# Performance work log

Measured on AMD Instinct MI355X. Metric: run time of the kernel, lower is better.

Reference implementation:

```python
import jax, jax.numpy as jnp
import numpy as np

COMMITMENT_COST = 0.25

def setup_inputs() -> dict:
    key = jax.random.key(0)
    k1, k2 = jax.random.split(key)
    z = jax.random.normal(k1, (8, 2048, 768), dtype=jnp.float32)
    # codebook initialized uniform(-1/K, 1/K) in the original; use same scale
    K = 2048
    emb = jax.random.uniform(k2, (K, 768), dtype=jnp.float32, minval=-1.0 / K, maxval=1.0 / K)
    return {"z": z, "emb": emb}

def reference(z, emb):
    B, S, D = z.shape
    z_flat = z.reshape(-1, D)                                   # [N, D]
    # squared-euclidean distances via expansion: ||z||^2 + ||e||^2 - 2 z e^T
    distances = (
        jnp.sum(z_flat * z_flat, axis=1, keepdims=True)
        + jnp.sum(emb * emb, axis=1)
        - 2.0 * jnp.matmul(z_flat, emb.T)
    )                                                           # [N, K]
    ids_flat = jnp.argmin(distances, axis=1)                    # [N]
    z_q = emb[ids_flat].reshape(z.shape)                        # gather + reshape
    concept_ids = ids_flat.reshape(B, S)
    # training path with use_ema=True: codebook_loss = 0, commitment term only.
    # NOTE: original (faithfully) computes mse(z.detach(), z_q) — grad flows to z_q.
    commitment_loss = jnp.mean((jax.lax.stop_gradient(z) - z_q) ** 2)
    vq_loss = COMMITMENT_COST * commitment_loss
    # straight-through estimator
    z_q_st = z + jax.lax.stop_gradient(z_q - z)
    return z_q_st, concept_ids, vq_loss
```

## Files before the change

kernel.cpp:

```cpp
#include <hip/hip_runtime.h>
#include <float.h>

typedef unsigned short ushort_t;
typedef unsigned int uint_t;

#define NROWS 16384
#define DDIM  768
#define KCODES 2048
#define MARGIN 8e-4f

__device__ __forceinline__ ushort_t f2bf(float x) {
    uint_t u = __float_as_uint(x);
    uint_t r = (u + 0x7fffu + ((u >> 16) & 1u)) >> 16;
    return (ushort_t)r;
}

__device__ __forceinline__ uint_t fenc(float f) {
    uint_t u = __float_as_uint(f);
    return (u & 0x80000000u) ? ~u : (u | 0x80000000u);
}
__device__ __forceinline__ float fdec(uint_t k) {
    uint_t u = (k & 0x80000000u) ? (k ^ 0x80000000u) : ~k;
    return __uint_as_float(u);
}

typedef __attribute__((ext_vector_type(8))) short bf16x8;
typedef __attribute__((ext_vector_type(8))) unsigned short ushort8;
typedef __attribute__((ext_vector_type(4))) float f32x4;

__device__ __forceinline__ int swz(int r) { return (r & 3) ^ ((r >> 2) & 3); }

__global__ void prep2_kernel(const float* __restrict__ emb, float* __restrict__ ee,
                             ushort_t* __restrict__ Eh, float* __restrict__ out_loss) {
    const int c = blockIdx.x, t = threadIdx.x;
    if (c == 0 && t == 0) out_loss[0] = 0.f;
    const float* e = emb + (size_t)c * DDIM;
    float s = 0.f;
    for (int i = t; i < DDIM; i += 256) { float v = e[i]; s += v * v; }
    for (int off = 32; off; off >>= 1) s += __shfl_down(s, off);
    __shared__ float red[4];
    if ((t & 63) == 0) red[t >> 6] = s;
    __syncthreads();
    if (t == 0) ee[c] = red[0] + red[1] + red[2] + red[3];
    if (t < 192) {
        const float4 v = ((const float4*)e)[t];
        ushort4 h;
        h.x = f2bf(v.x); h.y = f2bf(v.y); h.z = f2bf(v.z); h.w = f2bf(v.w);
        ((ushort4*)(Eh + (size_t)c * DDIM))[t] = h;
    }
}

#define R      64
#define CCH    512
#define NCH    4
#define KST    24
#define CAP    16
#define B_OFF    4096
#define RMIN_OFF 36864
#define RCNT_OFF 37120
#define SVAL_OFF 37376
#define SIDX_OFF 41472
#define LRED_OFF 45568
#define SMEM_SZ  45600

__global__ __launch_bounds__(256, 2)
void fused2_kernel(const float* __restrict__ z, const float* __restrict__ emb,
                   const ushort_t* __restrict__ Eh, const float* __restrict__ ee,
                   float* __restrict__ ids_f32, float* __restrict__ out0,
                   float* __restrict__ out_loss) {
    __shared__ __align__(16) char smem[SMEM_SZ];
    uint_t* rowminU = (uint_t*)(smem + RMIN_OFF);
    int*    rcnt    = (int*)(smem + RCNT_OFF);
    float (*sval)[CAP] = (float(*)[CAP])(smem + SVAL_OFF);
    int   (*sidx)[CAP] = (int(*)[CAP])(smem + SIDX_OFF);
    float*  lred    = (float*)(smem + LRED_OFF);

    const int t = threadIdx.x;
    const int w = t >> 6, l = t & 63;
    const int row0 = blockIdx.x * R;

    if (t < 64) { rowminU[t] = 0xFFFFFFFFu; rcnt[t] = 0; }

    const int arow = t >> 2, acs = t & 3;
    const float* zA = z + (size_t)(row0 + arow) * DDIM + acs * 8;
    char* aw = smem + (arow << 6) + ((acs ^ swz(arow)) << 4);

    const int sri = l >> 2, slot = l & 3;
    const int swzs = swz(sri);
    const int brow = w * 128 + sri;
    const uint_t lB = B_OFF + (uint_t)(w * 8192);

    const int g = l >> 4, lr = l & 15;
    int aoff[4], boff[8];
    #pragma unroll
    for (int mi = 0; mi < 4; ++mi) {
        const int r = mi * 16 + lr;
        aoff[mi] = (r << 6) + ((g ^ swz(r)) << 4);
    }
    #pragma unroll
    for (int ni = 0; ni < 8; ++ni) {
        const int rb = w * 128 + ni * 16 + lr;
        boff[ni] = B_OFF + (rb << 6) + ((g ^ swz(rb)) << 4);
    }

    f32x4 acc[4][8];
    for (int c = 0; c < NCH; ++c) {
        const int c0 = c * CCH;
        #pragma unroll
        for (int mi = 0; mi < 4; ++mi)
            #pragma unroll
            for (int ni = 0; ni < 8; ++ni) acc[mi][ni] = (f32x4){0.f, 0.f, 0.f, 0.f};

        const ushort_t* gB = Eh + (size_t)(c0 + brow) * DDIM + ((slot ^ swzs) << 3);

        for (int s = 0; s < KST; ++s) {
            __syncthreads();
            #pragma unroll
            for (int q = 0; q < 8; ++q)
                __builtin_amdgcn_global_load_lds(
                    (const __attribute__((address_space(1))) void*)(gB + q * (16 * DDIM)),
                    (__attribute__((address_space(3))) void*)(smem + lB + q * 1024),
                    16, 0, 0);
            {
                const float4 v0 = *(const float4*)(zA + 32 * s);
                const float4 v1 = *(const float4*)(zA + 32 * s + 4);
                ushort8 h;
                h[0] = f2bf(v0.x); h[1] = f2bf(v0.y); h[2] = f2bf(v0.z); h[3] = f2bf(v0.w);
                h[4] = f2bf(v1.x); h[5] = f2bf(v1.y); h[6] = f2bf(v1.z); h[7] = f2bf(v1.w);
                *(ushort8*)aw = h;
            }
            gB += 32;
            __syncthreads();

            bf16x8 af[4], bfr[8];
            #pragma unroll
            for (int mi = 0; mi < 4; ++mi) af[mi] = *(const bf16x8*)(smem + aoff[mi]);
            #pragma unroll
            for (int ni = 0; ni < 8; ++ni) bfr[ni] = *(const bf16x8*)(smem + boff[ni]);
            #pragma unroll
            for (int mi = 0; mi < 4; ++mi)
                #pragma unroll
                for (int ni = 0; ni < 8; ++ni)
                    acc[mi][ni] = __builtin_amdgcn_mfma_f32_16x16x32_bf16(
                        af[mi], bfr[ni], acc[mi][ni], 0, 0, 0);
        }

        float ecv[8];
        #pragma unroll
        for (int ni = 0; ni < 8; ++ni) ecv[ni] = ee[c0 + w * 128 + ni * 16 + lr];
        #pragma unroll
        for (int mi = 0; mi < 4; ++mi)
            #pragma unroll
            for (int ni = 0; ni < 8; ++ni)
                #pragma unroll
                for (int r = 0; r < 4; ++r)
                    acc[mi][ni][r] = ecv[ni] - 2.0f * acc[mi][ni][r];

        #pragma unroll
        for (int mi = 0; mi < 4; ++mi)
            #pragma unroll
            for (int r = 0; r < 4; ++r) {
                float v = acc[mi][0][r];
                #pragma unroll
                for (int ni = 1; ni < 8; ++ni) v = fminf(v, acc[mi][ni][r]);
                v = fminf(v, __shfl_xor(v, 1));
                v = fminf(v, __shfl_xor(v, 2));
                v = fminf(v, __shfl_xor(v, 4));
                v = fminf(v, __shfl_xor(v, 8));
                if (lr == 0) atomicMin(&rowminU[mi * 16 + g * 4 + r], fenc(v));
            }
        __syncthreads();
        #pragma unroll
        for (int mi = 0; mi < 4; ++mi)
            #pragma unroll
            for (int r = 0; r < 4; ++r) {
                const int lrow = mi * 16 + g * 4 + r;
                const float lim = fdec(rowminU[lrow]) + MARGIN;
                #pragma unroll
                for (int ni = 0; ni < 8; ++ni) {
                    const float vv = acc[mi][ni][r];
                    if (vv <= lim) {
                        const int p = atomicAdd(&rcnt[lrow], 1);
                        if (p < CAP) {
                            sval[lrow][p] = vv;
                            sidx[lrow][p] = c0 + w * 128 + ni * 16 + lr;
                        }
                    }
                }
            }
    }
    __syncthreads();

    float wloss = 0.f;
    for (int rr = 0; rr < 16; ++rr) {
        const int lrow = w * 16 + rr;
        const int row = row0 + lrow;
        const float* zr = z + (size_t)row * DDIM;

        float szz = 0.f;
        #pragma unroll
        for (int k = 0; k < 12; ++k) { const float v = zr[l + 64 * k]; szz += v * v; }
        for (int off = 32; off; off >>= 1) szz += __shfl_down(szz, off);
        const float zzr = __shfl(szz, 0);

        const float T = fdec(rowminU[lrow]) + MARGIN;
        const int n = rcnt[lrow] < CAP ? rcnt[lrow] : CAP;
        float val = FLT_MAX; int idx = 0x7fffffff;
        if (l < n) { val = sval[lrow][l]; idx = sidx[lrow][l]; }
        unsigned long long m = __ballot(val <= T);

        float bestd = FLT_MAX; int besti = 0x7fffffff;
        while (m) {
            const int j = __ffsll(m) - 1; m &= m - 1;
            const int cand = __shfl(idx, j);
            const float* er = emb + (size_t)cand * DDIM;
            float p = 0.f;
            #pragma unroll
            for (int k = 0; k < 12; ++k) p += zr[l + 64 * k] * er[l + 64 * k];
            for (int off = 32; off; off >>= 1) p += __shfl_down(p, off);
            if (l == 0) {
                const float t1 = zzr + ee[cand];
                const float d  = t1 - 2.0f * p;
                if (d < bestd || (d == bestd && cand < besti)) { bestd = d; besti = cand; }
            }
        }
        const int bi = __shfl(besti, 0);
        if (l == 0) ids_f32[row] = (float)bi;

        const float4* zr4 = (const float4*)zr;
        const float4* er4 = (const float4*)(emb + (size_t)bi * DDIM);
        float4* o4 = (float4*)(out0 + (size_t)row * DDIM);
        float s = 0.f;
        #pragma unroll
        for (int j2 = 0; j2 < 3; ++j2) {
            const int i4 = l + 64 * j2;
            const float4 zv = zr4[i4];
            const float4 ev = er4[i4];
            float4 o;
            o.x = zv.x + (ev.x - zv.x); o.y = zv.y + (ev.y - zv.y);
            o.z = zv.z + (ev.z - zv.z); o.w = zv.w + (ev.w - zv.w);
            o4[i4] = o;
            const float dx = zv.x - ev.x, dy = zv.y - ev.y;
            const float dz = zv.z - ev.z, dw = zv.w - ev.w;
            s += dx * dx + dy * dy + dz * dz + dw * dw;
        }
        for (int off = 32; off; off >>= 1) s += __shfl_down(s, off);
        if (l == 0) wloss += s;
    }
    if (l == 0) lred[w] = wloss;
    __syncthreads();
    if (t == 0) {
        float tot = lred[0] + lred[1] + lred[2] + lred[3];
        atomicAdd(out_loss, tot * (0.25f / (float)((size_t)NROWS * DDIM)));
    }
}

__global__ void ee_kernel(const float* __restrict__ emb, float* __restrict__ ee) {
    int c = blockIdx.x;
    const float* e = emb + (size_t)c * DDIM;
    int t = threadIdx.x;
    float s = 0.f;
    for (int i = t; i < DDIM; i += 256) { float v = e[i]; s += v * v; }
    for (int off = 32; off; off >>= 1) s += __shfl_down(s, off);
    __shared__ float red[4];
    if ((t & 63) == 0) red[t >> 6] = s;
    __syncthreads();
    if (t == 0) ee[c] = red[0] + red[1] + red[2] + red[3];
}

__global__ void zz_kernel(const float* __restrict__ z, float* __restrict__ zz) {
    const int t = threadIdx.x;
    const int row = blockIdx.x * 4 + (t >> 6);
    const int lane = t & 63;
    const float* zr = z + (size_t)row * DDIM;
    float s = 0.f;
    for (int i = lane; i < DDIM; i += 64) { float v = zr[i]; s += v * v; }
    for (int off = 32; off; off >>= 1) s += __shfl_down(s, off);
    if (lane == 0) zz[row] = s;
}

#define BM 32
#define BN 128
#define BKS 32
#define SPLITC 2
#define CODES_PER_BLOCK (KCODES / SPLITC)
#define NCHUNK (CODES_PER_BLOCK / BN)
#define NSTAGE (DDIM / BKS)
#define APADR 33
#define BPADC 132

__global__ __launch_bounds__(256)
void argmin_kernel(const float* __restrict__ z, const float* __restrict__ emb,
                   const float* __restrict__ ee, const float* __restrict__ zz,
                   float* __restrict__ pval, int* __restrict__ pidx) {
    __shared__ float Af[BKS][APADR];
    __shared__ float Bf[BKS][BPADC];
    __shared__ float cval[BM][33];
    __shared__ int   cidx[BM][33];
    __shared__ float zzs[BM];
    const int t = threadIdx.x;
    const int part = blockIdx.x & (SPLITC - 1);
    const int rb = blockIdx.x >> 1;
    const int row0 = rb * BM;
    const int cbase = part * CODES_PER_BLOCK;
    const int tx = t & 31, ty = t >> 5;
    const int sr = t >> 3;
    const int sk = 4 * (t & 7);
    if (t < BM) zzs[t] = zz[row0 + t];
    float bv[4]; int bi[4];
    #pragma unroll
    for (int i = 0; i < 4; ++i) { bv[i] = FLT_MAX; bi[i] = 0x7fffffff; }
    const float* zt = z + (size_t)(row0 + sr) * DDIM;
    for (int chunk = 0; chunk < NCHUNK; ++chunk) {
        const int c0 = cbase + chunk * BN;
        const float* ebase = emb + (size_t)(c0 + sr) * DDIM;
        float acc[4][4];
        #pragma unroll
        for (int i = 0; i < 4; ++i)
            #pragma unroll
            for (int j = 0; j < 4; ++j) acc[i][j] = 0.f;
        float4 pa = *(const float4*)&zt[sk];
        float4 pb[4];
        #pragma unroll
        for (int m = 0; m < 4; ++m) pb[m] = *(const float4*)&ebase[(size_t)(32 * m) * DDIM + sk];
        for (int s = 0; s < NSTAGE; ++s) {
            __syncthreads();
            Af[sk + 0][sr] = pa.x; Af[sk + 1][sr] = pa.y;
            Af[sk + 2][sr] = pa.z; Af[sk + 3][sr] = pa.w;
            #pragma unroll
            for (int m = 0; m < 4; ++m) {
                Bf[sk + 0][sr + 32 * m] = pb[m].x;
                Bf[sk + 1][sr + 32 * m] = pb[m].y;
                Bf[sk + 2][sr + 32 * m] = pb[m].z;
                Bf[sk + 3][sr + 32 * m] = pb[m].w;
            }
            __syncthreads();
            if (s + 1 < NSTAGE) {
                const int k1 = (s + 1) * BKS + sk;
                pa = *(const float4*)&zt[k1];
                #pragma unroll
                for (int m = 0; m < 4; ++m)
                    pb[m] = *(const float4*)&ebase[(size_t)(32 * m) * DDIM + k1];
            }
            #pragma unroll
            for (int kk = 0; kk < BKS; ++kk) {
                const float4 a4 = *(const float4*)&Af[kk][4 * ty];
                const float4 b4 = *(const float4*)&Bf[kk][4 * tx];
                const float aa[4] = {a4.x, a4.y, a4.z, a4.w};
                const float bb[4] = {b4.x, b4.y, b4.z, b4.w};
                #pragma unroll
                for (int i = 0; i < 4; ++i)
                    #pragma unroll
                    for (int j = 0; j < 4; ++j) acc[i][j] += aa[i] * bb[j];
            }
        }
        const float4 e4 = *(const float4*)&ee[c0 + 4 * tx];
        const float eev[4] = {e4.x, e4.y, e4.z, e4.w};
        #pragma unroll
        for (int i = 0; i < 4; ++i) {
            const float zzr = zzs[4 * ty + i];
            #pragma unroll
            for (int j = 0; j < 4; ++j) {
                const int code = c0 + 4 * tx + j;
                const float t1 = zzr + eev[j];
                const float d  = t1 - 2.0f * acc[i][j];
                if (d < bv[i] || (d == bv[i] && code < bi[i])) { bv[i] = d; bi[i] = code; }
            }
        }
    }
    __syncthreads();
    #pragma unroll
    for (int i = 0; i < 4; ++i) { cval[4 * ty + i][tx] = bv[i]; cidx[4 * ty + i][tx] = bi[i]; }
    __syncthreads();
    if (t < BM) {
        float v = FLT_MAX; int id = 0x7fffffff;
        #pragma unroll
        for (int x = 0; x < 32; ++x) {
            const float cv = cval[t][x]; const int ci = cidx[t][x];
            if (cv < v || (cv == v && ci < id)) { v = cv; id = ci; }
        }
        pval[part * NROWS + row0 + t] = v;
        pidx[part * NROWS + row0 + t] = id;
    }
}

__global__ void combine_kernel(const float* __restrict__ pval, const int* __restrict__ pidx,
                               float* __restrict__ ids_f32) {
    const int r = blockIdx.x * 256 + threadIdx.x;
    float v = pval[r];           int id = pidx[r];
    const float v1 = pval[NROWS + r]; const int i1 = pidx[NROWS + r];
    if (v1 < v || (v1 == v && i1 < id)) { v = v1; id = i1; }
    ids_f32[r] = (float)id;
}

__global__ __launch_bounds__(256)
void gather_kernel(const float* __restrict__ z, const float* __restrict__ emb,
                   const float* __restrict__ ids_f32, float* __restrict__ out0,
                   float* __restrict__ part) {
    const int b = blockIdx.x;
    const int t = threadIdx.x;
    const int rl = t >> 4, c = t & 15;
    __shared__ int ids[16];
    if (t < 16) ids[t] = (int)ids_f32[b * 16 + t];
    __syncthreads();
    const int row = b * 16 + rl;
    const float4* zr = (const float4*)(z + (size_t)row * DDIM);
    float4* orow = (float4*)(out0 + (size_t)row * DDIM);
    const float4* er = (const float4*)(emb + (size_t)ids[rl] * DDIM);
    float s = 0.f;
    #pragma unroll
    for (int j = 0; j < 12; ++j) {
        const int i4 = c + 16 * j;
        const float4 zv = zr[i4];
        const float4 ev = er[i4];
        float4 o;
        o.x = zv.x + (ev.x - zv.x); o.y = zv.y + (ev.y - zv.y);
        o.z = zv.z + (ev.z - zv.z); o.w = zv.w + (ev.w - zv.w);
        orow[i4] = o;
        float dx = zv.x - ev.x, dy = zv.y - ev.y, dz = zv.z - ev.z, dw = zv.w - ev.w;
        s += dx * dx + dy * dy + dz * dz + dw * dw;
    }
    for (int off = 32; off; off >>= 1) s += __shfl_down(s, off);
    __shared__ float red[4];
    if ((t & 63) == 0) red[t >> 6] = s;
    __syncthreads();
    if (t == 0) part[b] = red[0] + red[1] + red[2] + red[3];
}

__global__ void loss_kernel(const float* __restrict__ part, float* __restrict__ out_loss) {
    const int t = threadIdx.x;
    double s = 0.0;
    for (int i = t; i < 1024; i += 256) s += (double)part[i];
    for (int off = 32; off; off >>= 1) s += __shfl_down(s, off);
    __shared__ double red[4];
    if ((t & 63) == 0) red[t >> 6] = s;
    __syncthreads();
    if (t == 0) {
        const double total = red[0] + red[1] + red[2] + red[3];
        out_loss[0] = (float)(0.25 * (total / (double)((size_t)NROWS * DDIM)));
    }
}

#define EE_OFF   0
#define ZZ_OFF   8192
#define EH_OFF   73728
#define WS_NEED  (EH_OFF + (size_t)KCODES * DDIM * 2)
#define PART_OFF 73728
#define PV_OFF   81920

extern "C" void kernel_launch(void* const* d_in, const int* in_sizes, int n_in,
                              void* d_out, int out_size, void* d_ws, size_t ws_size,
                              hipStream_t stream) {
    const float* z   = (const float*)d_in[0];
    const float* emb = (const float*)d_in[1];

    float* out0     = (float*)d_out;
    float* out_ids  = out0 + (size_t)NROWS * DDIM;
    float* out_loss = out_ids + NROWS;

    char* ws = (char*)d_ws;
    float* ee   = (float*)(ws + EE_OFF);
    float* zzws = (float*)(ws + ZZ_OFF);

    if (ws_size >= WS_NEED) {
        ushort_t* Eh = (ushort_t*)(ws + EH_OFF);
        prep2_kernel<<<KCODES, 256, 0, stream>>>(emb, ee, Eh, out_loss);
        fused2_kernel<<<NROWS / R, 256, 0, stream>>>(z, emb, Eh, ee,
                                                     out_ids, out0, out_loss);
    } else {
        float* part = (float*)(ws + PART_OFF);
        float* pval = (float*)(ws + PV_OFF);
        int*   pidx = (int*)(ws + PV_OFF + 131072);
        ee_kernel<<<KCODES, 256, 0, stream>>>(emb, ee);
        zz_kernel<<<NROWS / 4, 256, 0, stream>>>(z, zzws);
        argmin_kernel<<<(NROWS / BM) * SPLITC, 256, 0, stream>>>(z, emb, ee, zzws, pval, pidx);
        combine_kernel<<<NROWS / 256, 256, 0, stream>>>(pval, pidx, out_ids);
        gather_kernel<<<NROWS / 16, 256, 0, stream>>>(z, emb, out_ids, out0, part);
        loss_kernel<<<1, 256, 0, stream>>>(part, out_loss);
    }
}
```

Before: 278.1 us.

## Split codebook across two blocks per row tile and add combine kernel

The fused kernel now handles half the codebook (two 512-code chunks) per block, launching 512 blocks instead of 256 so more CUs are occupied. Each block writes its per-row min and candidate slots to workspace, and a new combine kernel merges the two halves, rescores candidates in fp32, gathers, writes outputs and accumulates the loss. It trades an extra launch and workspace traffic, plus rereading z, for better GPU fill and a separate rescoring phase. The candidate threshold is now per half, so more candidates may be kept.

```diff
diff --git a/kernel.cpp b/kernel.cpp
--- a/kernel.cpp
+++ b/kernel.cpp
@@ -52,7 +52,7 @@
 
 #define R      64
 #define CCH    512
-#define NCH    4
+#define NCH    2
 #define KST    24
 #define CAP    16
 #define B_OFF    4096
@@ -60,24 +60,25 @@
 #define RCNT_OFF 37120
 #define SVAL_OFF 37376
 #define SIDX_OFF 41472
-#define LRED_OFF 45568
-#define SMEM_SZ  45600
+#define SMEM_SZ  45568
 
 __global__ __launch_bounds__(256, 2)
-void fused2_kernel(const float* __restrict__ z, const float* __restrict__ emb,
-                   const ushort_t* __restrict__ Eh, const float* __restrict__ ee,
-                   float* __restrict__ ids_f32, float* __restrict__ out0,
-                   float* __restrict__ out_loss) {
+void fused3_kernel(const float* __restrict__ z, const ushort_t* __restrict__ Eh,
+                   const float* __restrict__ ee, float* __restrict__ bmin,
+                   float2* __restrict__ slots) {
     __shared__ __align__(16) char smem[SMEM_SZ];
     uint_t* rowminU = (uint_t*)(smem + RMIN_OFF);
     int*    rcnt    = (int*)(smem + RCNT_OFF);
     float (*sval)[CAP] = (float(*)[CAP])(smem + SVAL_OFF);
     int   (*sidx)[CAP] = (int(*)[CAP])(smem + SIDX_OFF);
-    float*  lred    = (float*)(smem + LRED_OFF);
 
     const int t = threadIdx.x;
     const int w = t >> 6, l = t & 63;
-    const int row0 = blockIdx.x * R;
+    const int idx = blockIdx.x;
+    const int cb = (idx >> 3) & 1;
+    const int rb = (idx & 7) | ((idx >> 4) << 3);
+    const int row0 = rb * R;
+    const int codebase = cb * (NCH * CCH);
 
     if (t < 64) { rowminU[t] = 0xFFFFFFFFu; rcnt[t] = 0; }
 
@@ -99,13 +100,13 @@
     }
     #pragma unroll
     for (int ni = 0; ni < 8; ++ni) {
-        const int rb = w * 128 + ni * 16 + lr;
-        boff[ni] = B_OFF + (rb << 6) + ((g ^ swz(rb)) << 4);
+        const int rb2 = w * 128 + ni * 16 + lr;
+        boff[ni] = B_OFF + (rb2 << 6) + ((g ^ swz(rb2)) << 4);
     }
 
     f32x4 acc[4][8];
     for (int c = 0; c < NCH; ++c) {
-        const int c0 = c * CCH;
+        const int c0 = codebase + c * CCH;
         #pragma unroll
         for (int mi = 0; mi < 4; ++mi)
             #pragma unroll
@@ -191,66 +192,92 @@
     }
     __syncthreads();
 
-    float wloss = 0.f;
-    for (int rr = 0; rr < 16; ++rr) {
-        const int lrow = w * 16 + rr;
-        const int row = row0 + lrow;
-        const float* zr = z + (size_t)row * DDIM;
-
-        float szz = 0.f;
-        #pragma unroll
-        for (int k = 0; k < 12; ++k) { const float v = zr[l + 64 * k]; szz += v * v; }
-        for (int off = 32; off; off >>= 1) szz += __shfl_down(szz, off);
-        const float zzr = __shfl(szz, 0);
-
-        const float T = fdec(rowminU[lrow]) + MARGIN;
-        const int n = rcnt[lrow] < CAP ? rcnt[lrow] : CAP;
-        float val = FLT_MAX; int idx = 0x7fffffff;
-        if (l < n) { val = sval[lrow][l]; idx = sidx[lrow][l]; }
-        unsigned long long m = __ballot(val <= T);
-
-        float bestd = FLT_MAX; int besti = 0x7fffffff;
-        while (m) {
-            const int j = __ffsll(m) - 1; m &= m - 1;
-            const int cand = __shfl(idx, j);
-            const float* er = emb + (size_t)cand * DDIM;
-            float p = 0.f;
-            #pragma unroll
-            for (int k = 0; k < 12; ++k) p += zr[l + 64 * k] * er[l + 64 * k];
-            for (int off = 32; off; off >>= 1) p += __shfl_down(p, off);
-            if (l == 0) {
-                const float t1 = zzr + ee[cand];
-                const float d  = t1 - 2.0f * p;
-                if (d < bestd || (d == bestd && cand < besti)) { bestd = d; besti = cand; }
-            }
+    if (t < 64) bmin[(size_t)cb * NROWS + row0 + t] = fdec(rowminU[t]);
+    {
+        const int rr = t >> 2, qp = t & 3;
+        const int n = rcnt[rr] < CAP ? rcnt[rr] : CAP;
+        const int s0 = qp * 4;
+        float v0 = (s0 + 0 < n) ? sval[rr][s0 + 0] : FLT_MAX;
+        float v1 = (s0 + 1 < n) ? sval[rr][s0 + 1] : FLT_MAX;
+        float v2 = (s0 + 2 < n) ? sval[rr][s0 + 2] : FLT_MAX;
+        float v3 = (s0 + 3 < n) ? sval[rr][s0 + 3] : FLT_MAX;
+        int i0 = (s0 + 0 < n) ? sidx[rr][s0 + 0] : 0x7fffffff;
+        int i1 = (s0 + 1 < n) ? sidx[rr][s0 + 1] : 0x7fffffff;
+        int i2 = (s0 + 2 < n) ? sidx[rr][s0 + 2] : 0x7fffffff;
+        int i3 = (s0 + 3 < n) ? sidx[rr][s0 + 3] : 0x7fffffff;
+        float4* dst = (float4*)(slots + ((size_t)cb * NROWS + row0 + rr) * CAP) + qp * 2;
+        dst[0] = make_float4(v0, __int_as_float(i0), v1, __int_as_float(i1));
+        dst[1] = make_float4(v2, __int_as_float(i2), v3, __int_as_float(i3));
+    }
+}
+
+__global__ __launch_bounds__(256)
+void combine2_kernel(const float* __restrict__ bmin, const float2* __restrict__ slots,
+                     const float* __restrict__ ee, const float* __restrict__ z,
+                     const float* __restrict__ emb, float* __restrict__ ids_f32,
+                     float* __restrict__ out0, float* __restrict__ out_loss) {
+    const int t = threadIdx.x;
+    const int w = t >> 6;
+    const int row = blockIdx.x * 4 + w;
+    const int l = t & 63;
+
+    float v = (l < 2) ? bmin[(size_t)l * NROWS + row] : FLT_MAX;
+    v = fminf(v, __shfl_xor(v, 1));
+    const float T = __shfl(v, 0) + MARGIN;
+
+    float2 a = make_float2(FLT_MAX, __int_as_float(0x7fffffff));
+    if (l < 32) a = slots[((size_t)(l >> 4) * NROWS + row) * CAP + (l & 15)];
+    unsigned long long m = __ballot(a.x <= T);
+
+    const float* zr = z + (size_t)row * DDIM;
+
+    float szz = 0.f;
+    #pragma unroll
+    for (int k = 0; k < 12; ++k) { const float vz = zr[l + 64 * k]; szz += vz * vz; }
+    for (int off = 32; off; off >>= 1) szz += __shfl_down(szz, off);
+    const float zzr = __shfl(szz, 0);
+
+    float bestd = FLT_MAX; int besti = 0x7fffffff;
+    while (m) {
+        const int j = __ffsll(m) - 1; m &= m - 1;
+        const int cand = __float_as_int(__shfl(a.y, j));
+        const float* er = emb + (size_t)cand * DDIM;
+        float p = 0.f;
+        #pragma unroll
+        for (int k = 0; k < 12; ++k) p += zr[l + 64 * k] * er[l + 64 * k];
+        for (int off = 32; off; off >>= 1) p += __shfl_down(p, off);
+        if (l == 0) {
+            const float t1 = zzr + ee[cand];
+            const float d  = t1 - 2.0f * p;
+            if (d < bestd || (d == bestd && cand < besti)) { bestd = d; besti = cand; }
         }
-        const int bi = __shfl(besti, 0);
-        if (l == 0) ids_f32[row] = (float)bi;
-
-        const float4* zr4 = (const float4*)zr;
-        const float4* er4 = (const float4*)(emb + (size_t)bi * DDIM);
-        float4* o4 = (float4*)(out0 + (size_t)row * DDIM);
-        float s = 0.f;
-        #pragma unroll
-        for (int j2 = 0; j2 < 3; ++j2) {
-            const int i4 = l + 64 * j2;
-            const float4 zv = zr4[i4];
-            const float4 ev = er4[i4];
-            float4 o;
-            o.x = zv.x + (ev.x - zv.x); o.y = zv.y + (ev.y - zv.y);
-            o.z = zv.z + (ev.z - zv.z); o.w = zv.w + (ev.w - zv.w);
-            o4[i4] = o;
-            const float dx = zv.x - ev.x, dy = zv.y - ev.y;
-            const float dz = zv.z - ev.z, dw = zv.w - ev.w;
-            s += dx * dx + dy * dy + dz * dz + dw * dw;
-        }
-        for (int off = 32; off; off >>= 1) s += __shfl_down(s, off);
-        if (l == 0) wloss += s;
-    }
-    if (l == 0) lred[w] = wloss;
+    }
+    const int bi = __shfl(besti, 0);
+    if (l == 0) ids_f32[row] = (float)bi;
+
+    const float4* zr4 = (const float4*)zr;
+    const float4* er4 = (const float4*)(emb + (size_t)bi * DDIM);
+    float4* o4 = (float4*)(out0 + (size_t)row * DDIM);
+    float s = 0.f;
+    #pragma unroll
+    for (int j = 0; j < 3; ++j) {
+        const int i4 = l + 64 * j;
+        const float4 zv = zr4[i4];
+        const float4 ev = er4[i4];
+        float4 o;
+        o.x = zv.x + (ev.x - zv.x); o.y = zv.y + (ev.y - zv.y);
+        o.z = zv.z + (ev.z - zv.z); o.w = zv.w + (ev.w - zv.w);
+        o4[i4] = o;
+        const float dx = zv.x - ev.x, dy = zv.y - ev.y;
+        const float dz = zv.z - ev.z, dw = zv.w - ev.w;
+        s += dx * dx + dy * dy + dz * dz + dw * dw;
+    }
+    for (int off = 32; off; off >>= 1) s += __shfl_down(s, off);
+    __shared__ float lred[4];
+    if (l == 0) lred[w] = s;
     __syncthreads();
     if (t == 0) {
-        float tot = lred[0] + lred[1] + lred[2] + lred[3];
+        const float tot = lred[0] + lred[1] + lred[2] + lred[3];
         atomicAdd(out_loss, tot * (0.25f / (float)((size_t)NROWS * DDIM)));
     }
 }
@@ -444,7 +471,9 @@
 #define EE_OFF   0
 #define ZZ_OFF   8192
 #define EH_OFF   73728
-#define WS_NEED  (EH_OFF + (size_t)KCODES * DDIM * 2)
+#define BMIN_OFF (EH_OFF + (size_t)KCODES * DDIM * 2)
+#define SLOT_OFF (BMIN_OFF + (size_t)2 * NROWS * 4)
+#define WS_NEED  (SLOT_OFF + (size_t)2 * NROWS * CAP * 8)
 #define PART_OFF 73728
 #define PV_OFF   81920
 
@@ -463,10 +492,13 @@
     float* zzws = (float*)(ws + ZZ_OFF);
 
     if (ws_size >= WS_NEED) {
-        ushort_t* Eh = (ushort_t*)(ws + EH_OFF);
+        ushort_t* Eh   = (ushort_t*)(ws + EH_OFF);
+        float*    bmin = (float*)(ws + BMIN_OFF);
+        float2*   slot = (float2*)(ws + SLOT_OFF);
         prep2_kernel<<<KCODES, 256, 0, stream>>>(emb, ee, Eh, out_loss);
-        fused2_kernel<<<NROWS / R, 256, 0, stream>>>(z, emb, Eh, ee,
-                                                     out_ids, out0, out_loss);
+        fused3_kernel<<<512, 256, 0, stream>>>(z, Eh, ee, bmin, slot);
+        combine2_kernel<<<NROWS / 4, 256, 0, stream>>>(bmin, slot, ee, z, emb,
+                                                       out_ids, out0, out_loss);
     } else {
         float* part = (float*)(ws + PART_OFF);
         float* pval = (float*)(ws + PV_OFF);
```

Measured after the change: 242.9 us. -12.7%, faster.
